# Optimization experiments

Hardware: AMD Instinct MI355X
Metric: run time of the kernel (lower is better)

The kernel has to match this reference:

```python
import jax, jax.numpy as jnp
import numpy as np

BN_EPS = 1e-5


def _spe_forward(feature, neigh_idx, W, gamma, beta, running_mean, running_var):
    # feature: [B, C, N, 1]; neigh_idx: [B, N, K]
    B = feature.shape[0]
    pc = jnp.transpose(feature[..., 0], (0, 2, 1))            # [B, N, C]
    # gather neighbor features: [B, N, K, C]
    f_neigh = pc[jnp.arange(B)[:, None, None], neigh_idx]
    f_neigh = jnp.transpose(f_neigh, (0, 3, 1, 2))            # [B, C, N, K]
    f = jnp.concatenate((feature, f_neigh), axis=-1)          # [B, C, N, K+1]
    # 1x1 conv (no bias, followed by BN)
    h = jnp.einsum('oc,bcnk->bonk', W, f)                     # [B, O, N, K+1]
    # BatchNorm2d (eval mode with running stats) + ReLU
    inv = gamma / jnp.sqrt(running_var + BN_EPS)
    h = h * inv[None, :, None, None] + (beta - running_mean * inv)[None, :, None, None]
    h = jax.nn.relu(h)
    # sum over the neighbor axis, keepdim
    return jnp.sum(h, axis=-1, keepdims=True)                 # [B, O, N, 1]


def setup_inputs() -> dict:
    key = jax.random.key(0)
    k1, k2, k3 = jax.random.split(key, 3)
    B, C, N, K, O = 2, 64, 32768, 16, 64
    feature = jax.random.normal(k1, (B, C, N, 1), dtype=jnp.float32)
    neigh_idx = jax.random.randint(k2, (B, N, K), 0, N, dtype=jnp.int32)
    W = jax.random.normal(k3, (O, C), dtype=jnp.float32) * (1.0 / np.sqrt(C))
    gamma = jnp.ones((O,), dtype=jnp.float32)
    beta = jnp.zeros((O,), dtype=jnp.float32)
    running_mean = jnp.zeros((O,), dtype=jnp.float32)
    running_var = jnp.ones((O,), dtype=jnp.float32)
    return {"feature": feature, "neigh_idx": neigh_idx, "W": W,
            "gamma": gamma, "beta": beta,
            "running_mean": running_mean, "running_var": running_var}


def reference(feature, neigh_idx, W, gamma, beta, running_mean, running_var):
    return _spe_forward(feature, neigh_idx, W, gamma, beta, running_mean, running_var)
```

## Files before the change

kernel.cpp:

```cpp
#include <hip/hip_runtime.h>

#define BN_EPS 1e-5f

constexpr int Bb = 2;
constexpr int Cc = 64;
constexpr int Nn = 32768;
constexpr int Kk = 16;
constexpr int Oo = 64;

typedef __attribute__((ext_vector_type(8))) short v8s;
typedef __attribute__((ext_vector_type(4))) float v4f;

__device__ __forceinline__ unsigned short f2bf(float f) {
    unsigned u = __float_as_uint(f);
    return (unsigned short)((u + 0x7FFFu + ((u >> 16) & 1u)) >> 16);
}

__global__ __launch_bounds__(256) void spe_gemm_mfma(
    const float* __restrict__ feature, const float* __restrict__ W,
    const float* __restrict__ gamma, const float* __restrict__ beta,
    const float* __restrict__ rmean, const float* __restrict__ rvar,
    unsigned short* __restrict__ t)
{
    const int tid = threadIdx.x;
    const int blk = blockIdx.x;
    const int b   = blk & 1;
    const int n0  = (blk >> 1) << 6;

    const int wv   = tid >> 6;
    const int lane = tid & 63;
    const int q    = lane >> 4;
    const int r16  = lane & 15;

    union U { ushort4 u4[2]; unsigned short us[8]; v8s v; };

    const int nb = n0 + wv * 16 + r16;
    const float* fp = feature + (size_t)b * Cc * Nn + nb;
    U bf0, bf1;
    #pragma unroll
    for (int jj = 0; jj < 8; ++jj) {
        bf0.us[jj] = f2bf(fp[(size_t)(q * 8 + jj) * Nn]);
        bf1.us[jj] = f2bf(fp[(size_t)(q * 8 + jj + 32) * Nn]);
    }

    #pragma unroll
    for (int ot = 0; ot < 4; ++ot) {
        const int oa = ot * 16 + r16;
        const float* wp = W + oa * 64 + q * 8;
        U af0, af1;
        #pragma unroll
        for (int jj = 0; jj < 8; ++jj) {
            af0.us[jj] = f2bf(wp[jj]);
            af1.us[jj] = f2bf(wp[jj + 32]);
        }
        v4f c = {0.f, 0.f, 0.f, 0.f};
        c = __builtin_amdgcn_mfma_f32_16x16x32_bf16(af0.v, bf0.v, c, 0, 0, 0);
        c = __builtin_amdgcn_mfma_f32_16x16x32_bf16(af1.v, bf1.v, c, 0, 0, 0);

        const int ob4 = ot * 16 + q * 4;
        const float4 g4  = *(const float4*)&gamma[ob4];
        const float4 be4 = *(const float4*)&beta[ob4];
        const float4 m4  = *(const float4*)&rmean[ob4];
        const float4 v4  = *(const float4*)&rvar[ob4];
        float inv[4], bias[4];
        inv[0] = g4.x / sqrtf(v4.x + BN_EPS);  bias[0] = be4.x - m4.x * inv[0];
        inv[1] = g4.y / sqrtf(v4.y + BN_EPS);  bias[1] = be4.y - m4.y * inv[1];
        inv[2] = g4.z / sqrtf(v4.z + BN_EPS);  bias[2] = be4.z - m4.z * inv[2];
        inv[3] = g4.w / sqrtf(v4.w + BN_EPS);  bias[3] = be4.w - m4.w * inv[3];

        ushort4 ov;
        ov.x = f2bf(fmaxf(fmaf(inv[0], c[0], bias[0]), 0.0f));
        ov.y = f2bf(fmaxf(fmaf(inv[1], c[1], bias[1]), 0.0f));
        ov.z = f2bf(fmaxf(fmaf(inv[2], c[2], bias[2]), 0.0f));
        ov.w = f2bf(fmaxf(fmaf(inv[3], c[3], bias[3]), 0.0f));
        *(ushort4*)&t[((size_t)b * Nn + nb) * 64 + ob4] = ov;
    }
}

__global__ __launch_bounds__(512, 4) void spe_gather_sum(
    const unsigned short* __restrict__ t, const int* __restrict__ idx,
    float* __restrict__ out)
{
    __shared__ float s[64 * 65];
    const int tid  = threadIdx.x;
    const int wv   = tid >> 6;
    const int lane = tid & 63;
    const int p    = lane >> 3;
    const int e    = lane & 7;
    const int blk  = blockIdx.x;
    const int b    = blk & 1;
    const int n0   = (blk >> 1) << 6;
    const int ng   = n0 + wv * 8;

    const unsigned short* tb = t + (size_t)b * Nn * 64;

    const int2 mi = ((const int2*)(idx + ((size_t)b * Nn + ng) * Kk))[lane];

    const int n = ng + p;
    uint4 v[17];
    v[0] = *(const uint4*)&tb[(size_t)n * 64 + e * 8];
    #pragma unroll
    for (int j = 0; j < 16; ++j) {
        const int src = p * 8 + (j >> 1);
        const int nj  = __shfl((j & 1) ? mi.y : mi.x, src);
        v[j + 1] = *(const uint4*)&tb[(size_t)nj * 64 + e * 8];
    }

    float acc[8] = {0.f, 0.f, 0.f, 0.f, 0.f, 0.f, 0.f, 0.f};
    #pragma unroll
    for (int j = 0; j < 17; ++j) {
        acc[0] += __uint_as_float(v[j].x << 16);
        acc[1] += __uint_as_float(v[j].x & 0xFFFF0000u);
        acc[2] += __uint_as_float(v[j].y << 16);
        acc[3] += __uint_as_float(v[j].y & 0xFFFF0000u);
        acc[4] += __uint_as_float(v[j].z << 16);
        acc[5] += __uint_as_float(v[j].z & 0xFFFF0000u);
        acc[6] += __uint_as_float(v[j].w << 16);
        acc[7] += __uint_as_float(v[j].w & 0xFFFF0000u);
    }

    float* sp = &s[(wv * 8 + p) * 65 + e * 8];
    #pragma unroll
    for (int i = 0; i < 8; ++i) sp[i] = acc[i];
    __syncthreads();

    const int nl2 = tid & 63;
    const int ob  = tid >> 6;
    float* op = out + (size_t)b * Oo * Nn + n0 + nl2;
    #pragma unroll
    for (int i = 0; i < 8; ++i) {
        const int o = ob * 8 + i;
        op[(size_t)o * Nn] = s[nl2 * 65 + o];
    }
}

extern "C" void kernel_launch(void* const* d_in, const int* in_sizes, int n_in,
                              void* d_out, int out_size, void* d_ws, size_t ws_size,
                              hipStream_t stream) {
    const float* feature = (const float*)d_in[0];
    const int*   nidx    = (const int*)d_in[1];
    const float* W       = (const float*)d_in[2];
    const float* gamma   = (const float*)d_in[3];
    const float* beta    = (const float*)d_in[4];
    const float* rmean   = (const float*)d_in[5];
    const float* rvar    = (const float*)d_in[6];
    float* out = (float*)d_out;
    unsigned short* t = (unsigned short*)d_ws;

    const int nblocks = Bb * (Nn / 64);
    spe_gemm_mfma<<<nblocks, 256, 0, stream>>>(feature, W, gamma, beta, rmean, rvar, t);
    spe_gather_sum<<<nblocks, 512, 0, stream>>>(t, nidx, out);
}
```

Before: 100.5 us.

## Stage bf16 weights in LDS and widen gather kernel to 1024 threads

The GEMM kernel now converts W to bf16 once per block into shared memory and reads MFMA A-fragments from LDS, instead of having every wave reload and convert W from global memory. The gather-sum kernel doubles its block to 1024 threads, so each lane gathers 8-byte ushort4 slices instead of 16-byte chunks, with each wave covering 4 points. The neighbour indices are broadcast by shuffle from a single int per lane. This is meant to raise memory-level parallelism for the random gathers. The cost is smaller per-lane transactions and a larger block with a __syncthreads barrier.

```diff
diff --git a/kernel.cpp b/kernel.cpp
--- a/kernel.cpp
+++ b/kernel.cpp
@@ -15,6 +15,9 @@
     unsigned u = __float_as_uint(f);
     return (unsigned short)((u + 0x7FFFu + ((u >> 16) & 1u)) >> 16);
 }
+__device__ __forceinline__ float bf2f(unsigned short h) {
+    return __uint_as_float(((unsigned)h) << 16);
+}
 
 __global__ __launch_bounds__(256) void spe_gemm_mfma(
     const float* __restrict__ feature, const float* __restrict__ W,
@@ -22,10 +25,17 @@
     const float* __restrict__ rmean, const float* __restrict__ rvar,
     unsigned short* __restrict__ t)
 {
+    __shared__ unsigned short Wl[64][68];
     const int tid = threadIdx.x;
     const int blk = blockIdx.x;
     const int b   = blk & 1;
     const int n0  = (blk >> 1) << 6;
+
+    #pragma unroll
+    for (int j = 0; j < 16; ++j) {
+        const int i = j * 256 + tid;
+        Wl[i >> 6][i & 63] = f2bf(W[i]);
+    }
 
     const int wv   = tid >> 6;
     const int lane = tid & 63;
@@ -42,17 +52,17 @@
         bf0.us[jj] = f2bf(fp[(size_t)(q * 8 + jj) * Nn]);
         bf1.us[jj] = f2bf(fp[(size_t)(q * 8 + jj + 32) * Nn]);
     }
+    __syncthreads();
 
     #pragma unroll
     for (int ot = 0; ot < 4; ++ot) {
         const int oa = ot * 16 + r16;
-        const float* wp = W + oa * 64 + q * 8;
         U af0, af1;
-        #pragma unroll
-        for (int jj = 0; jj < 8; ++jj) {
-            af0.us[jj] = f2bf(wp[jj]);
-            af1.us[jj] = f2bf(wp[jj + 32]);
-        }
+        af0.u4[0] = *(const ushort4*)&Wl[oa][q * 8];
+        af0.u4[1] = *(const ushort4*)&Wl[oa][q * 8 + 4];
+        af1.u4[0] = *(const ushort4*)&Wl[oa][q * 8 + 32];
+        af1.u4[1] = *(const ushort4*)&Wl[oa][q * 8 + 36];
+
         v4f c = {0.f, 0.f, 0.f, 0.f};
         c = __builtin_amdgcn_mfma_f32_16x16x32_bf16(af0.v, bf0.v, c, 0, 0, 0);
         c = __builtin_amdgcn_mfma_f32_16x16x32_bf16(af1.v, bf1.v, c, 0, 0, 0);
@@ -77,7 +87,7 @@
     }
 }
 
-__global__ __launch_bounds__(512, 4) void spe_gather_sum(
+__global__ __launch_bounds__(1024, 4) void spe_gather_sum(
     const unsigned short* __restrict__ t, const int* __restrict__ idx,
     float* __restrict__ out)
 {
@@ -85,51 +95,44 @@
     const int tid  = threadIdx.x;
     const int wv   = tid >> 6;
     const int lane = tid & 63;
-    const int p    = lane >> 3;
-    const int e    = lane & 7;
+    const int p    = lane >> 4;
+    const int q    = lane & 15;
     const int blk  = blockIdx.x;
     const int b    = blk & 1;
     const int n0   = (blk >> 1) << 6;
-    const int ng   = n0 + wv * 8;
+    const int ng   = n0 + wv * 4;
 
     const unsigned short* tb = t + (size_t)b * Nn * 64;
 
-    const int2 mi = ((const int2*)(idx + ((size_t)b * Nn + ng) * Kk))[lane];
+    const int myidx = idx[((size_t)b * Nn + ng) * Kk + lane];
 
-    const int n = ng + p;
-    uint4 v[17];
-    v[0] = *(const uint4*)&tb[(size_t)n * 64 + e * 8];
+    int nj[16];
     #pragma unroll
-    for (int j = 0; j < 16; ++j) {
-        const int src = p * 8 + (j >> 1);
-        const int nj  = __shfl((j & 1) ? mi.y : mi.x, src);
-        v[j + 1] = *(const uint4*)&tb[(size_t)nj * 64 + e * 8];
+    for (int j = 0; j < 16; ++j) nj[j] = __shfl(myidx, p * 16 + j);
+
+    ushort4 v[17];
+    v[0] = *(const ushort4*)&tb[(size_t)(ng + p) * 64 + q * 4];
+    #pragma unroll
+    for (int j = 0; j < 16; ++j)
+        v[j + 1] = *(const ushort4*)&tb[(size_t)nj[j] * 64 + q * 4];
+
+    float ax = 0.f, ay = 0.f, az = 0.f, aw = 0.f;
+    #pragma unroll
+    for (int j = 0; j < 17; ++j) {
+        ax += bf2f(v[j].x); ay += bf2f(v[j].y);
+        az += bf2f(v[j].z); aw += bf2f(v[j].w);
     }
 
-    float acc[8] = {0.f, 0.f, 0.f, 0.f, 0.f, 0.f, 0.f, 0.f};
-    #pragma unroll
-    for (int j = 0; j < 17; ++j) {
-        acc[0] += __uint_as_float(v[j].x << 16);
-        acc[1] += __uint_as_float(v[j].x & 0xFFFF0000u);
-        acc[2] += __uint_as_float(v[j].y << 16);
-        acc[3] += __uint_as_float(v[j].y & 0xFFFF0000u);
-        acc[4] += __uint_as_float(v[j].z << 16);
-        acc[5] += __uint_as_float(v[j].z & 0xFFFF0000u);
-        acc[6] += __uint_as_float(v[j].w << 16);
-        acc[7] += __uint_as_float(v[j].w & 0xFFFF0000u);
-    }
-
-    float* sp = &s[(wv * 8 + p) * 65 + e * 8];
-    #pragma unroll
-    for (int i = 0; i < 8; ++i) sp[i] = acc[i];
+    float* sp = &s[(wv * 4 + p) * 65 + q * 4];
+    sp[0] = ax; sp[1] = ay; sp[2] = az; sp[3] = aw;
     __syncthreads();
 
     const int nl2 = tid & 63;
     const int ob  = tid >> 6;
     float* op = out + (size_t)b * Oo * Nn + n0 + nl2;
     #pragma unroll
-    for (int i = 0; i < 8; ++i) {
-        const int o = ob * 8 + i;
+    for (int i = 0; i < 4; ++i) {
+        const int o = ob * 4 + i;
         op[(size_t)o * Nn] = s[nl2 * 65 + o];
     }
 }
@@ -149,5 +152,5 @@
 
     const int nblocks = Bb * (Nn / 64);
     spe_gemm_mfma<<<nblocks, 256, 0, stream>>>(feature, W, gamma, beta, rmean, rvar, t);
-    spe_gather_sum<<<nblocks, 512, 0, stream>>>(t, nidx, out);
+    spe_gather_sum<<<nblocks, 1024, 0, stream>>>(t, nidx, out);
 }
```

Measured after the change: 95.25 us. 1.06x faster.
